# Optimization experiments

Measured on AMD Instinct MI355X. Metric: run time of the kernel, lower is better.

Reference implementation:

```python
import jax, jax.numpy as jnp
import numpy as np

N = 262144      # nodes per graph
NC = 65536      # common nodes
D = 256         # feature_dim


def setup_inputs() -> dict:
    key = jax.random.key(0)
    ks = jax.random.split(key, 12)
    h_prop = jax.random.normal(ks[0], (N, D), dtype=jnp.float32)
    h_context = jax.random.normal(ks[1], (N, D), dtype=jnp.float32)
    h_orig = jax.random.normal(ks[2], (NC, D), dtype=jnp.float32)
    # unique indices (torch scatter-assign semantics are only well-defined without dups)
    idx_prop = jnp.sort(jax.random.permutation(ks[3], N)[:NC]).astype(jnp.int64)
    idx_ctx = jnp.sort(jax.random.permutation(ks[4], N)[:NC]).astype(jnp.int64)
    # parameters (xavier-ish scale)
    s = 1.0 / np.sqrt(D)
    w_orig = jax.random.normal(ks[5], (D, D), dtype=jnp.float32) * s
    w_prop = jax.random.normal(ks[6], (D, D), dtype=jnp.float32) * s
    w_ctx = jax.random.normal(ks[7], (D, D), dtype=jnp.float32) * s
    W_fuse = jax.random.normal(ks[8], (D, 3 * D), dtype=jnp.float32) * (1.0 / np.sqrt(3 * D))  # torch Linear weight (out,in)
    b_fuse = jnp.zeros((D,), dtype=jnp.float32)
    bias = jax.random.uniform(ks[9], (D,), dtype=jnp.float32, minval=-s, maxval=s)
    return {
        "h_prop": h_prop, "h_context": h_context,
        "h_original_common_nodes": h_orig,
        "w_orig": w_orig, "w_prop": w_prop, "w_ctx": w_ctx,
        "W_fuse": W_fuse, "b_fuse": b_fuse, "bias": bias,
        "common_node_indices_in_prop": idx_prop,
        "common_node_indices_in_context": idx_ctx,
    }


def reference(h_prop, h_context, h_original_common_nodes,
              w_orig, w_prop, w_ctx, W_fuse, b_fuse, bias,
              common_node_indices_in_prop, common_node_indices_in_context):
    # gather common rows + three small GEMMs  [NC, D]
    t_orig = h_original_common_nodes @ w_orig
    t_prop = h_prop[common_node_indices_in_prop] @ w_prop
    t_ctx = h_context[common_node_indices_in_context] @ w_ctx
    # concat-linear-tanh-bias  [NC, D]
    fused = jnp.concatenate([t_orig, t_prop, t_ctx], axis=1) @ W_fuse.T + b_fuse
    fused = jnp.tanh(fused) + bias
    # scatter update into clones of the full tables
    h_prop_updated = h_prop.at[common_node_indices_in_prop].set(fused)
    h_context_updated = h_context.at[common_node_indices_in_context].set(fused)
    return (h_prop_updated, h_context_updated)
```

## Files before the change

kernel.cpp:

```cpp
#include <hip/hip_runtime.h>
#include <hip/hip_bf16.h>

#define NN 262144
#define NCC 65536
#define DD 256

typedef __bf16 bf16x8 __attribute__((ext_vector_type(8)));
typedef float f32x4 __attribute__((ext_vector_type(4)));

__global__ void k_zero16(unsigned char* p, int n16) {
    int i = blockIdx.x * blockDim.x + threadIdx.x;
    if (i < n16) ((uint4*)p)[i] = make_uint4(0u, 0u, 0u, 0u);
}

__global__ void k_setflags(const int* __restrict__ idxp, const int* __restrict__ idxc,
                           unsigned char* fp, unsigned char* fc) {
    int j = blockIdx.x * blockDim.x + threadIdx.x;
    if (j < NCC) { fp[idxp[j]] = 1; fc[idxc[j]] = 1; }
}

__global__ __launch_bounds__(256) void k_precompute(const float* __restrict__ w_orig,
                                                    const float* __restrict__ w_prop,
                                                    const float* __restrict__ w_ctx,
                                                    const float* __restrict__ W_fuse,
                                                    __bf16* __restrict__ Mt) {
    int b = blockIdx.x;
    int seg = b >> 4, rem = b & 15;
    int ot = rem >> 2, mt = rem & 3;
    const float* wseg = seg == 0 ? w_orig : (seg == 1 ? w_prop : w_ctx);
    __shared__ float Wl[64 * 65];
    __shared__ float wl[64 * 65];
    int t = threadIdx.x;
    int to = (t & 15) * 4, tm = (t >> 4) * 4;
    float acc[4][4] = {};
    for (int kc = 0; kc < 4; ++kc) {
        __syncthreads();
        for (int i = 0; i < 16; ++i) {
            int f = i * 256 + t;
            int row = f >> 6, col = f & 63;
            Wl[row * 65 + col] = W_fuse[(size_t)(ot * 64 + row) * 768 + seg * 256 + kc * 64 + col];
            wl[row * 65 + col] = wseg[(size_t)(mt * 64 + row) * 256 + kc * 64 + col];
        }
        __syncthreads();
        for (int k = 0; k < 64; ++k) {
            float wo[4], wm2[4];
#pragma unroll
            for (int i = 0; i < 4; ++i) wo[i] = Wl[(to + i) * 65 + k];
#pragma unroll
            for (int j = 0; j < 4; ++j) wm2[j] = wl[(tm + j) * 65 + k];
#pragma unroll
            for (int i = 0; i < 4; ++i)
#pragma unroll
                for (int j = 0; j < 4; ++j) acc[i][j] += wo[i] * wm2[j];
        }
    }
    for (int i = 0; i < 4; ++i)
        for (int j = 0; j < 4; ++j) {
            int o = ot * 64 + to + i;
            int g = seg * 256 + mt * 64 + tm + j;
            Mt[(size_t)o * 768 + g] = (__bf16)acc[i][j];
        }
}

__global__ __launch_bounds__(512, 4) void k_gemm(const float* __restrict__ hp,
                                                 const float* __restrict__ hc,
                                                 const float* __restrict__ horig,
                                                 const __bf16* __restrict__ Mt,
                                                 const float* __restrict__ bfuse,
                                                 const float* __restrict__ bias,
                                                 const int* __restrict__ idxp,
                                                 const int* __restrict__ idxc,
                                                 float* __restrict__ out0,
                                                 float* __restrict__ out1) {
    __shared__ __bf16 Al[64 * 64];
    __shared__ __bf16 Bl[256 * 64];
    int t = threadIdx.x;
    int jbase = blockIdx.x * 64;
    int lane = t & 63, wid = t >> 6;
    int wm = wid >> 2, wn = wid & 3;

    int ar = t >> 3;
    int aslot = t & 7;
    int jr = jbase + ar;
    const float* rowp0 = horig + (size_t)jr * 256;
    const float* rowp1 = hp + (size_t)idxp[jr] * 256;
    const float* rowp2 = hc + (size_t)idxc[jr] * 256;

    int bo = t >> 1;
    int bkp = t & 1;

    f32x4 acc[2][4] = {};

    for (int c = 0; c < 12; ++c) {
        if (c) __syncthreads();
        {
            int seg = c >> 2, ko = (c & 3) * 64;
            const float* src = (seg == 0 ? rowp0 : (seg == 1 ? rowp1 : rowp2)) + ko + aslot * 8;
            float4 v0 = *(const float4*)(src);
            float4 v1 = *(const float4*)(src + 4);
            bf16x8 w;
            w[0] = (__bf16)v0.x; w[1] = (__bf16)v0.y; w[2] = (__bf16)v0.z; w[3] = (__bf16)v0.w;
            w[4] = (__bf16)v1.x; w[5] = (__bf16)v1.y; w[6] = (__bf16)v1.z; w[7] = (__bf16)v1.w;
            *(bf16x8*)&Al[ar * 64 + ((aslot ^ (ar & 7)) << 3)] = w;
        }
        {
            const __bf16* src = Mt + (size_t)bo * 768 + c * 64 + bkp * 32;
#pragma unroll
            for (int i = 0; i < 4; ++i) {
                bf16x8 v = *(const bf16x8*)(src + i * 8);
                int slot = bkp * 4 + i;
                *(bf16x8*)&Bl[bo * 64 + ((slot ^ (bo & 7)) << 3)] = v;
            }
        }
        __syncthreads();
#pragma unroll
        for (int ks = 0; ks < 2; ++ks) {
            bf16x8 af[2], bfr[4];
            int kslot = ks * 4 + (lane >> 4);
#pragma unroll
            for (int mi = 0; mi < 2; ++mi) {
                int r = wm * 32 + mi * 16 + (lane & 15);
                af[mi] = *(const bf16x8*)&Al[r * 64 + ((kslot ^ (r & 7)) << 3)];
            }
#pragma unroll
            for (int ni = 0; ni < 4; ++ni) {
                int o = wn * 64 + ni * 16 + (lane & 15);
                bfr[ni] = *(const bf16x8*)&Bl[o * 64 + ((kslot ^ (o & 7)) << 3)];
            }
#pragma unroll
            for (int mi = 0; mi < 2; ++mi)
#pragma unroll
                for (int ni = 0; ni < 4; ++ni)
                    acc[mi][ni] = __builtin_amdgcn_mfma_f32_16x16x32_bf16(af[mi], bfr[ni], acc[mi][ni], 0, 0, 0);
        }
    }

    float bfv[4], biv[4];
#pragma unroll
    for (int ni = 0; ni < 4; ++ni) {
        int o = wn * 64 + ni * 16 + (lane & 15);
        bfv[ni] = bfuse[o];
        biv[ni] = bias[o];
    }
#pragma unroll
    for (int mi = 0; mi < 2; ++mi) {
#pragma unroll
        for (int rr = 0; rr < 4; ++rr) {
            int j = jbase + wm * 32 + mi * 16 + (lane >> 4) * 4 + rr;
            int gp = idxp[j];
            int gc = idxc[j];
#pragma unroll
            for (int ni = 0; ni < 4; ++ni) {
                int o = wn * 64 + ni * 16 + (lane & 15);
                float v = tanhf(acc[mi][ni][rr] + bfv[ni]) + biv[ni];
                out0[(size_t)gp * 256 + o] = v;
                out1[(size_t)gc * 256 + o] = v;
            }
        }
    }
}

__global__ __launch_bounds__(256) void k_copy(const float* __restrict__ hp,
                                              const float* __restrict__ hc,
                                              const unsigned char* __restrict__ fp,
                                              const unsigned char* __restrict__ fc,
                                              float* __restrict__ out0,
                                              float* __restrict__ out1) {
    int wid = (blockIdx.x * blockDim.x + threadIdx.x) >> 6;
    int lane = threadIdx.x & 63;
    int nw = (gridDim.x * blockDim.x) >> 6;
    for (int R = wid; R < 2 * NN; R += nw) {
        int tbl = (R >= NN);
        int r = tbl ? (R - NN) : R;
        unsigned char f = tbl ? fc[r] : fp[r];
        if (!f) {
            const float* s = (tbl ? hc : hp) + (size_t)r * 256 + lane * 4;
            float* d = (tbl ? out1 : out0) + (size_t)r * 256 + lane * 4;
            *(float4*)d = *(const float4*)s;
        }
    }
}

extern "C" void kernel_launch(void* const* d_in, const int* in_sizes, int n_in,
                              void* d_out, int out_size, void* d_ws, size_t ws_size,
                              hipStream_t stream) {
    const float* hp     = (const float*)d_in[0];
    const float* hc     = (const float*)d_in[1];
    const float* horig  = (const float*)d_in[2];
    const float* w_orig = (const float*)d_in[3];
    const float* w_prop = (const float*)d_in[4];
    const float* w_ctx  = (const float*)d_in[5];
    const float* W_fuse = (const float*)d_in[6];
    const float* bfuse  = (const float*)d_in[7];
    const float* bias   = (const float*)d_in[8];
    const int* idxp     = (const int*)d_in[9];
    const int* idxc     = (const int*)d_in[10];
    float* out0 = (float*)d_out;
    float* out1 = out0 + (size_t)NN * DD;

    char* ws = (char*)d_ws;
    __bf16* Mt = (__bf16*)ws;
    unsigned char* fp = (unsigned char*)(ws + 393216);
    unsigned char* fc = fp + NN;

    k_zero16<<<(2 * NN / 16 + 255) / 256, 256, 0, stream>>>(fp, 2 * NN / 16);
    k_setflags<<<NCC / 256, 256, 0, stream>>>(idxp, idxc, fp, fc);
    k_precompute<<<48, 256, 0, stream>>>(w_orig, w_prop, w_ctx, W_fuse, Mt);
    k_gemm<<<NCC / 64, 512, 0, stream>>>(hp, hc, horig, Mt, bfuse, bias, idxp, idxc, out0, out1);
    k_copy<<<4096, 256, 0, stream>>>(hp, hc, fp, fc, out0, out1);
}
```

Before: 334.6 us.

## Fuse GEMM and copy kernels, load MFMA operands directly from global

Merges the flag zeroing into the weight precompute kernel, and fuses the GEMM with the unflagged-row copy in a single 1024-block kernel. Odd blocks copy first and even blocks compute first, so copy traffic overlaps with compute. The GEMM drops its LDS staging and barriers, and each wave loads its A rows (converted to bf16) and its B fragments straight from global memory. This saves launches and synchronisation, but waves now load B redundantly and read A in a less coalesced pattern.

New measurement: 447.1 us. 33.6% more time.

```diff
diff --git a/kernel.cpp b/kernel.cpp
--- a/kernel.cpp
+++ b/kernel.cpp
@@ -1,36 +1,30 @@
 #include <hip/hip_runtime.h>
 #include <hip/hip_bf16.h>
+#include <math.h>
 
 #define NN 262144
 #define NCC 65536
-#define DD 256
 
 typedef __bf16 bf16x8 __attribute__((ext_vector_type(8)));
 typedef float f32x4 __attribute__((ext_vector_type(4)));
 
-__global__ void k_zero16(unsigned char* p, int n16) {
-    int i = blockIdx.x * blockDim.x + threadIdx.x;
-    if (i < n16) ((uint4*)p)[i] = make_uint4(0u, 0u, 0u, 0u);
-}
-
-__global__ void k_setflags(const int* __restrict__ idxp, const int* __restrict__ idxc,
-                           unsigned char* fp, unsigned char* fc) {
-    int j = blockIdx.x * blockDim.x + threadIdx.x;
-    if (j < NCC) { fp[idxp[j]] = 1; fc[idxc[j]] = 1; }
-}
-
-__global__ __launch_bounds__(256) void k_precompute(const float* __restrict__ w_orig,
-                                                    const float* __restrict__ w_prop,
-                                                    const float* __restrict__ w_ctx,
-                                                    const float* __restrict__ W_fuse,
-                                                    __bf16* __restrict__ Mt) {
+__global__ __launch_bounds__(256) void k_setup(const float* __restrict__ w_orig,
+                                               const float* __restrict__ w_prop,
+                                               const float* __restrict__ w_ctx,
+                                               const float* __restrict__ W_fuse,
+                                               __bf16* __restrict__ Mt,
+                                               unsigned char* __restrict__ flags) {
+    __shared__ float Wl[64 * 65];
+    __shared__ float wl[64 * 65];
     int b = blockIdx.x;
+    int t = threadIdx.x;
+    if (b >= 48) {
+        ((uint4*)flags)[(b - 48) * 256 + t] = make_uint4(0u, 0u, 0u, 0u);
+        return;
+    }
     int seg = b >> 4, rem = b & 15;
     int ot = rem >> 2, mt = rem & 3;
     const float* wseg = seg == 0 ? w_orig : (seg == 1 ? w_prop : w_ctx);
-    __shared__ float Wl[64 * 65];
-    __shared__ float wl[64 * 65];
-    int t = threadIdx.x;
     int to = (t & 15) * 4, tm = (t >> 4) * 4;
     float acc[4][4] = {};
     for (int kc = 0; kc < 4; ++kc) {
@@ -62,83 +56,110 @@
         }
 }
 
-__global__ __launch_bounds__(512, 4) void k_gemm(const float* __restrict__ hp,
-                                                 const float* __restrict__ hc,
-                                                 const float* __restrict__ horig,
-                                                 const __bf16* __restrict__ Mt,
-                                                 const float* __restrict__ bfuse,
-                                                 const float* __restrict__ bias,
-                                                 const int* __restrict__ idxp,
-                                                 const int* __restrict__ idxc,
-                                                 float* __restrict__ out0,
-                                                 float* __restrict__ out1) {
-    __shared__ __bf16 Al[64 * 64];
-    __shared__ __bf16 Bl[256 * 64];
+__global__ void k_setflags(const int* __restrict__ idxp, const int* __restrict__ idxc,
+                           unsigned char* fp, unsigned char* fc) {
+    int j = blockIdx.x * blockDim.x + threadIdx.x;
+    if (j < NCC) { fp[idxp[j]] = 1; fc[idxc[j]] = 1; }
+}
+
+__device__ inline bf16x8 cvt8(f32x4 a, f32x4 b) {
+    bf16x8 w;
+    w[0] = (__bf16)a[0]; w[1] = (__bf16)a[1]; w[2] = (__bf16)a[2]; w[3] = (__bf16)a[3];
+    w[4] = (__bf16)b[0]; w[5] = (__bf16)b[1]; w[6] = (__bf16)b[2]; w[7] = (__bf16)b[3];
+    return w;
+}
+
+__device__ inline void do_copy(int bx, int wid, int lane,
+                               const float* __restrict__ hp, const float* __restrict__ hc,
+                               const unsigned char* __restrict__ fp,
+                               const unsigned char* __restrict__ fc,
+                               float* __restrict__ out0, float* __restrict__ out1) {
+    int base = bx * 512 + wid * 64;
+    int tbl = base >= NN;
+    const unsigned char* F = tbl ? fc : fp;
+    const float* S = tbl ? hc : hp;
+    float* D = tbl ? out1 : out0;
+    int r0 = tbl ? base - NN : base;
+    for (int i = 0; i < 64; ++i) {
+        int r = r0 + i;
+        if (!F[r]) {
+            const float* s = S + (size_t)r * 256 + lane * 4;
+            float* d = D + (size_t)r * 256 + lane * 4;
+            *(f32x4*)d = *(const f32x4*)s;
+        }
+    }
+}
+
+__global__ __launch_bounds__(512) void k_fused(const float* __restrict__ hp,
+                                               const float* __restrict__ hc,
+                                               const float* __restrict__ horig,
+                                               const __bf16* __restrict__ Mt,
+                                               const float* __restrict__ bfuse,
+                                               const float* __restrict__ bias,
+                                               const int* __restrict__ idxp,
+                                               const int* __restrict__ idxc,
+                                               const unsigned char* __restrict__ fp,
+                                               const unsigned char* __restrict__ fc,
+                                               float* __restrict__ out0,
+                                               float* __restrict__ out1) {
     int t = threadIdx.x;
-    int jbase = blockIdx.x * 64;
     int lane = t & 63, wid = t >> 6;
     int wm = wid >> 2, wn = wid & 3;
-
-    int ar = t >> 3;
-    int aslot = t & 7;
-    int jr = jbase + ar;
-    const float* rowp0 = horig + (size_t)jr * 256;
-    const float* rowp1 = hp + (size_t)idxp[jr] * 256;
-    const float* rowp2 = hc + (size_t)idxc[jr] * 256;
-
-    int bo = t >> 1;
-    int bkp = t & 1;
+    int jbase = blockIdx.x * 64;
+    int l15 = lane & 15, lq = lane >> 4;
+
+    int copyFirst = blockIdx.x & 1;
+    if (copyFirst) do_copy(blockIdx.x, wid, lane, hp, hc, fp, fc, out0, out1);
+
+    int j0 = jbase + wm * 32 + l15;
+    int j1 = j0 + 16;
+    int ip0 = idxp[j0], ip1 = idxp[j1];
+    int ic0 = idxc[j0], ic1 = idxc[j1];
+
+    const __bf16* bp0 = Mt + (size_t)(wn * 64 + 0  + l15) * 768 + lq * 8;
+    const __bf16* bp1 = Mt + (size_t)(wn * 64 + 16 + l15) * 768 + lq * 8;
+    const __bf16* bp2 = Mt + (size_t)(wn * 64 + 32 + l15) * 768 + lq * 8;
+    const __bf16* bp3 = Mt + (size_t)(wn * 64 + 48 + l15) * 768 + lq * 8;
 
     f32x4 acc[2][4] = {};
 
-    for (int c = 0; c < 12; ++c) {
-        if (c) __syncthreads();
-        {
-            int seg = c >> 2, ko = (c & 3) * 64;
-            const float* src = (seg == 0 ? rowp0 : (seg == 1 ? rowp1 : rowp2)) + ko + aslot * 8;
-            float4 v0 = *(const float4*)(src);
-            float4 v1 = *(const float4*)(src + 4);
-            bf16x8 w;
-            w[0] = (__bf16)v0.x; w[1] = (__bf16)v0.y; w[2] = (__bf16)v0.z; w[3] = (__bf16)v0.w;
-            w[4] = (__bf16)v1.x; w[5] = (__bf16)v1.y; w[6] = (__bf16)v1.z; w[7] = (__bf16)v1.w;
-            *(bf16x8*)&Al[ar * 64 + ((aslot ^ (ar & 7)) << 3)] = w;
-        }
-        {
-            const __bf16* src = Mt + (size_t)bo * 768 + c * 64 + bkp * 32;
-#pragma unroll
-            for (int i = 0; i < 4; ++i) {
-                bf16x8 v = *(const bf16x8*)(src + i * 8);
-                int slot = bkp * 4 + i;
-                *(bf16x8*)&Bl[bo * 64 + ((slot ^ (bo & 7)) << 3)] = v;
+#pragma unroll
+    for (int seg = 0; seg < 3; ++seg) {
+        const float* a0 = (seg == 0 ? horig + (size_t)j0 * 256
+                          : seg == 1 ? hp + (size_t)ip0 * 256
+                                     : hc + (size_t)ic0 * 256) + lq * 8;
+        const float* a1 = (seg == 0 ? horig + (size_t)j1 * 256
+                          : seg == 1 ? hp + (size_t)ip1 * 256
+                                     : hc + (size_t)ic1 * 256) + lq * 8;
+#pragma unroll
+        for (int cc = 0; cc < 4; ++cc) {
+            int c = seg * 4 + cc;
+#pragma unroll
+            for (int ks = 0; ks < 2; ++ks) {
+                int aoff = cc * 64 + ks * 32;
+                int boff = c * 64 + ks * 32;
+                bf16x8 af0 = cvt8(*(const f32x4*)(a0 + aoff), *(const f32x4*)(a0 + aoff + 4));
+                bf16x8 af1 = cvt8(*(const f32x4*)(a1 + aoff), *(const f32x4*)(a1 + aoff + 4));
+                bf16x8 b0 = *(const bf16x8*)(bp0 + boff);
+                bf16x8 b1 = *(const bf16x8*)(bp1 + boff);
+                bf16x8 b2 = *(const bf16x8*)(bp2 + boff);
+                bf16x8 b3 = *(const bf16x8*)(bp3 + boff);
+                acc[0][0] = __builtin_amdgcn_mfma_f32_16x16x32_bf16(af0, b0, acc[0][0], 0, 0, 0);
+                acc[0][1] = __builtin_amdgcn_mfma_f32_16x16x32_bf16(af0, b1, acc[0][1], 0, 0, 0);
+                acc[0][2] = __builtin_amdgcn_mfma_f32_16x16x32_bf16(af0, b2, acc[0][2], 0, 0, 0);
+                acc[0][3] = __builtin_amdgcn_mfma_f32_16x16x32_bf16(af0, b3, acc[0][3], 0, 0, 0);
+                acc[1][0] = __builtin_amdgcn_mfma_f32_16x16x32_bf16(af1, b0, acc[1][0], 0, 0, 0);
+                acc[1][1] = __builtin_amdgcn_mfma_f32_16x16x32_bf16(af1, b1, acc[1][1], 0, 0, 0);
+                acc[1][2] = __builtin_amdgcn_mfma_f32_16x16x32_bf16(af1, b2, acc[1][2], 0, 0, 0);
+                acc[1][3] = __builtin_amdgcn_mfma_f32_16x16x32_bf16(af1, b3, acc[1][3], 0, 0, 0);
             }
         }
-        __syncthreads();
-#pragma unroll
-        for (int ks = 0; ks < 2; ++ks) {
-            bf16x8 af[2], bfr[4];
-            int kslot = ks * 4 + (lane >> 4);
-#pragma unroll
-            for (int mi = 0; mi < 2; ++mi) {
-                int r = wm * 32 + mi * 16 + (lane & 15);
-                af[mi] = *(const bf16x8*)&Al[r * 64 + ((kslot ^ (r & 7)) << 3)];
-            }
-#pragma unroll
-            for (int ni = 0; ni < 4; ++ni) {
-                int o = wn * 64 + ni * 16 + (lane & 15);
-                bfr[ni] = *(const bf16x8*)&Bl[o * 64 + ((kslot ^ (o & 7)) << 3)];
-            }
-#pragma unroll
-            for (int mi = 0; mi < 2; ++mi)
-#pragma unroll
-                for (int ni = 0; ni < 4; ++ni)
-                    acc[mi][ni] = __builtin_amdgcn_mfma_f32_16x16x32_bf16(af[mi], bfr[ni], acc[mi][ni], 0, 0, 0);
-        }
     }
 
     float bfv[4], biv[4];
 #pragma unroll
     for (int ni = 0; ni < 4; ++ni) {
-        int o = wn * 64 + ni * 16 + (lane & 15);
+        int o = wn * 64 + ni * 16 + l15;
         bfv[ni] = bfuse[o];
         biv[ni] = bias[o];
     }
@@ -146,39 +167,20 @@
     for (int mi = 0; mi < 2; ++mi) {
 #pragma unroll
         for (int rr = 0; rr < 4; ++rr) {
-            int j = jbase + wm * 32 + mi * 16 + (lane >> 4) * 4 + rr;
+            int j = jbase + wm * 32 + mi * 16 + lq * 4 + rr;
             int gp = idxp[j];
             int gc = idxc[j];
 #pragma unroll
             for (int ni = 0; ni < 4; ++ni) {
-                int o = wn * 64 + ni * 16 + (lane & 15);
+                int o = wn * 64 + ni * 16 + l15;
                 float v = tanhf(acc[mi][ni][rr] + bfv[ni]) + biv[ni];
                 out0[(size_t)gp * 256 + o] = v;
                 out1[(size_t)gc * 256 + o] = v;
             }
         }
     }
-}
-
-__global__ __launch_bounds__(256) void k_copy(const float* __restrict__ hp,
-                                              const float* __restrict__ hc,
-                                              const unsigned char* __restrict__ fp,
-                                              const unsigned char* __restrict__ fc,
-                                              float* __restrict__ out0,
-                                              float* __restrict__ out1) {
-    int wid = (blockIdx.x * blockDim.x + threadIdx.x) >> 6;
-    int lane = threadIdx.x & 63;
-    int nw = (gridDim.x * blockDim.x) >> 6;
-    for (int R = wid; R < 2 * NN; R += nw) {
-        int tbl = (R >= NN);
-        int r = tbl ? (R - NN) : R;
-        unsigned char f = tbl ? fc[r] : fp[r];
-        if (!f) {
-            const float* s = (tbl ? hc : hp) + (size_t)r * 256 + lane * 4;
-            float* d = (tbl ? out1 : out0) + (size_t)r * 256 + lane * 4;
-            *(float4*)d = *(const float4*)s;
-        }
-    }
+
+    if (!copyFirst) do_copy(blockIdx.x, wid, lane, hp, hc, fp, fc, out0, out1);
 }
 
 extern "C" void kernel_launch(void* const* d_in, const int* in_sizes, int n_in,
@@ -196,16 +198,15 @@
     const int* idxp     = (const int*)d_in[9];
     const int* idxc     = (const int*)d_in[10];
     float* out0 = (float*)d_out;
-    float* out1 = out0 + (size_t)NN * DD;
+    float* out1 = out0 + (size_t)NN * 256;
 
     char* ws = (char*)d_ws;
     __bf16* Mt = (__bf16*)ws;
     unsigned char* fp = (unsigned char*)(ws + 393216);
     unsigned char* fc = fp + NN;
 
-    k_zero16<<<(2 * NN / 16 + 255) / 256, 256, 0, stream>>>(fp, 2 * NN / 16);
+    k_setup<<<176, 256, 0, stream>>>(w_orig, w_prop, w_ctx, W_fuse, Mt, fp);
     k_setflags<<<NCC / 256, 256, 0, stream>>>(idxp, idxc, fp, fc);
-    k_precompute<<<48, 256, 0, stream>>>(w_orig, w_prop, w_ctx, W_fuse, Mt);
-    k_gemm<<<NCC / 64, 512, 0, stream>>>(hp, hc, horig, Mt, bfuse, bias, idxp, idxc, out0, out1);
-    k_copy<<<4096, 256, 0, stream>>>(hp, hc, fp, fc, out0, out1);
-}
+    k_fused<<<1024, 512, 0, stream>>>(hp, hc, horig, Mt, bfuse, bias,
+                                      idxp, idxc, fp, fc, out0, out1);
+}
```

## Prefetch next GEMM tile into registers, merge setup kernels, unroll copy loop

Applied to the files above, without the earlier changes.

The GEMM kernel now loads the next k-chunk of A and B into registers while the current chunk is being stored to shared memory, so global-load latency overlaps with the MFMA work. Flag zeroing is folded into the weight-precompute kernel as extra blocks, which removes one kernel launch. The copy kernel becomes a fixed, unrolled 32-iteration loop that always issues its load (redirected to row 0 for flagged rows) to raise memory-level parallelism. The costs are higher register pressure in the GEMM and redundant loads of row 0 in the copy kernel.

Result: faster. 323.7 us (-3.3%).

```diff
diff --git a/kernel.cpp b/kernel.cpp
--- a/kernel.cpp
+++ b/kernel.cpp
@@ -1,36 +1,30 @@
 #include <hip/hip_runtime.h>
 #include <hip/hip_bf16.h>
+#include <math.h>
 
 #define NN 262144
 #define NCC 65536
-#define DD 256
 
 typedef __bf16 bf16x8 __attribute__((ext_vector_type(8)));
 typedef float f32x4 __attribute__((ext_vector_type(4)));
 
-__global__ void k_zero16(unsigned char* p, int n16) {
-    int i = blockIdx.x * blockDim.x + threadIdx.x;
-    if (i < n16) ((uint4*)p)[i] = make_uint4(0u, 0u, 0u, 0u);
-}
-
-__global__ void k_setflags(const int* __restrict__ idxp, const int* __restrict__ idxc,
-                           unsigned char* fp, unsigned char* fc) {
-    int j = blockIdx.x * blockDim.x + threadIdx.x;
-    if (j < NCC) { fp[idxp[j]] = 1; fc[idxc[j]] = 1; }
-}
-
-__global__ __launch_bounds__(256) void k_precompute(const float* __restrict__ w_orig,
-                                                    const float* __restrict__ w_prop,
-                                                    const float* __restrict__ w_ctx,
-                                                    const float* __restrict__ W_fuse,
-                                                    __bf16* __restrict__ Mt) {
+__global__ __launch_bounds__(256) void k_setup(const float* __restrict__ w_orig,
+                                               const float* __restrict__ w_prop,
+                                               const float* __restrict__ w_ctx,
+                                               const float* __restrict__ W_fuse,
+                                               __bf16* __restrict__ Mt,
+                                               unsigned char* __restrict__ flags) {
+    __shared__ float Wl[64 * 65];
+    __shared__ float wl[64 * 65];
     int b = blockIdx.x;
+    int t = threadIdx.x;
+    if (b >= 48) {
+        ((uint4*)flags)[(b - 48) * 256 + t] = make_uint4(0u, 0u, 0u, 0u);
+        return;
+    }
     int seg = b >> 4, rem = b & 15;
     int ot = rem >> 2, mt = rem & 3;
     const float* wseg = seg == 0 ? w_orig : (seg == 1 ? w_prop : w_ctx);
-    __shared__ float Wl[64 * 65];
-    __shared__ float wl[64 * 65];
-    int t = threadIdx.x;
     int to = (t & 15) * 4, tm = (t >> 4) * 4;
     float acc[4][4] = {};
     for (int kc = 0; kc < 4; ++kc) {
@@ -60,6 +54,19 @@
             int g = seg * 256 + mt * 64 + tm + j;
             Mt[(size_t)o * 768 + g] = (__bf16)acc[i][j];
         }
+}
+
+__global__ void k_setflags(const int* __restrict__ idxp, const int* __restrict__ idxc,
+                           unsigned char* fp, unsigned char* fc) {
+    int j = blockIdx.x * blockDim.x + threadIdx.x;
+    if (j < NCC) { fp[idxp[j]] = 1; fc[idxc[j]] = 1; }
+}
+
+__device__ inline bf16x8 cvt8(f32x4 a, f32x4 b) {
+    bf16x8 w;
+    w[0] = (__bf16)a[0]; w[1] = (__bf16)a[1]; w[2] = (__bf16)a[2]; w[3] = (__bf16)a[3];
+    w[4] = (__bf16)b[0]; w[5] = (__bf16)b[1]; w[6] = (__bf16)b[2]; w[7] = (__bf16)b[3];
+    return w;
 }
 
 __global__ __launch_bounds__(512, 4) void k_gemm(const float* __restrict__ hp,
@@ -78,53 +85,56 @@
     int jbase = blockIdx.x * 64;
     int lane = t & 63, wid = t >> 6;
     int wm = wid >> 2, wn = wid & 3;
-
-    int ar = t >> 3;
-    int aslot = t & 7;
+    int l15 = lane & 15, lq = lane >> 4;
+
+    int ar = t >> 3, aslot = t & 7;
     int jr = jbase + ar;
-    const float* rowp0 = horig + (size_t)jr * 256;
-    const float* rowp1 = hp + (size_t)idxp[jr] * 256;
-    const float* rowp2 = hc + (size_t)idxc[jr] * 256;
-
-    int bo = t >> 1;
-    int bkp = t & 1;
+    const float* rowp0 = horig + (size_t)jr * 256 + aslot * 8;
+    const float* rowp1 = hp + (size_t)idxp[jr] * 256 + aslot * 8;
+    const float* rowp2 = hc + (size_t)idxc[jr] * 256 + aslot * 8;
+
+    int bo = t >> 1, bkp = t & 1;
+    const __bf16* bsrc = Mt + (size_t)bo * 768 + bkp * 32;
 
     f32x4 acc[2][4] = {};
 
+    f32x4 va0 = *(const f32x4*)(rowp0);
+    f32x4 va1 = *(const f32x4*)(rowp0 + 4);
+    bf16x8 vb[4];
+#pragma unroll
+    for (int i = 0; i < 4; ++i) vb[i] = *(const bf16x8*)(bsrc + i * 8);
+
+#pragma unroll
     for (int c = 0; c < 12; ++c) {
-        if (c) __syncthreads();
-        {
-            int seg = c >> 2, ko = (c & 3) * 64;
-            const float* src = (seg == 0 ? rowp0 : (seg == 1 ? rowp1 : rowp2)) + ko + aslot * 8;
-            float4 v0 = *(const float4*)(src);
-            float4 v1 = *(const float4*)(src + 4);
-            bf16x8 w;
-            w[0] = (__bf16)v0.x; w[1] = (__bf16)v0.y; w[2] = (__bf16)v0.z; w[3] = (__bf16)v0.w;
-            w[4] = (__bf16)v1.x; w[5] = (__bf16)v1.y; w[6] = (__bf16)v1.z; w[7] = (__bf16)v1.w;
-            *(bf16x8*)&Al[ar * 64 + ((aslot ^ (ar & 7)) << 3)] = w;
-        }
-        {
-            const __bf16* src = Mt + (size_t)bo * 768 + c * 64 + bkp * 32;
-#pragma unroll
-            for (int i = 0; i < 4; ++i) {
-                bf16x8 v = *(const bf16x8*)(src + i * 8);
-                int slot = bkp * 4 + i;
-                *(bf16x8*)&Bl[bo * 64 + ((slot ^ (bo & 7)) << 3)] = v;
-            }
+        __syncthreads();
+        *(bf16x8*)&Al[ar * 64 + ((aslot ^ (ar & 7)) << 3)] = cvt8(va0, va1);
+#pragma unroll
+        for (int i = 0; i < 4; ++i) {
+            int slot = bkp * 4 + i;
+            *(bf16x8*)&Bl[bo * 64 + ((slot ^ (bo & 7)) << 3)] = vb[i];
+        }
+        if (c < 11) {
+            int cn = c + 1;
+            int seg = cn >> 2, ko = (cn & 3) * 64;
+            const float* s = (seg == 0 ? rowp0 : (seg == 1 ? rowp1 : rowp2)) + ko;
+            va0 = *(const f32x4*)(s);
+            va1 = *(const f32x4*)(s + 4);
+#pragma unroll
+            for (int i = 0; i < 4; ++i) vb[i] = *(const bf16x8*)(bsrc + cn * 64 + i * 8);
         }
         __syncthreads();
 #pragma unroll
         for (int ks = 0; ks < 2; ++ks) {
             bf16x8 af[2], bfr[4];
-            int kslot = ks * 4 + (lane >> 4);
+            int kslot = ks * 4 + lq;
 #pragma unroll
             for (int mi = 0; mi < 2; ++mi) {
-                int r = wm * 32 + mi * 16 + (lane & 15);
+                int r = wm * 32 + mi * 16 + l15;
                 af[mi] = *(const bf16x8*)&Al[r * 64 + ((kslot ^ (r & 7)) << 3)];
             }
 #pragma unroll
             for (int ni = 0; ni < 4; ++ni) {
-                int o = wn * 64 + ni * 16 + (lane & 15);
+                int o = wn * 64 + ni * 16 + l15;
                 bfr[ni] = *(const bf16x8*)&Bl[o * 64 + ((kslot ^ (o & 7)) << 3)];
             }
 #pragma unroll
@@ -138,7 +148,7 @@
     float bfv[4], biv[4];
 #pragma unroll
     for (int ni = 0; ni < 4; ++ni) {
-        int o = wn * 64 + ni * 16 + (lane & 15);
+        int o = wn * 64 + ni * 16 + l15;
         bfv[ni] = bfuse[o];
         biv[ni] = bias[o];
     }
@@ -146,12 +156,12 @@
     for (int mi = 0; mi < 2; ++mi) {
 #pragma unroll
         for (int rr = 0; rr < 4; ++rr) {
-            int j = jbase + wm * 32 + mi * 16 + (lane >> 4) * 4 + rr;
+            int j = jbase + wm * 32 + mi * 16 + lq * 4 + rr;
             int gp = idxp[j];
             int gc = idxc[j];
 #pragma unroll
             for (int ni = 0; ni < 4; ++ni) {
-                int o = wn * 64 + ni * 16 + (lane & 15);
+                int o = wn * 64 + ni * 16 + l15;
                 float v = tanhf(acc[mi][ni][rr] + bfv[ni]) + biv[ni];
                 out0[(size_t)gp * 256 + o] = v;
                 out1[(size_t)gc * 256 + o] = v;
@@ -166,18 +176,21 @@
                                               const unsigned char* __restrict__ fc,
                                               float* __restrict__ out0,
                                               float* __restrict__ out1) {
-    int wid = (blockIdx.x * blockDim.x + threadIdx.x) >> 6;
-    int lane = threadIdx.x & 63;
-    int nw = (gridDim.x * blockDim.x) >> 6;
-    for (int R = wid; R < 2 * NN; R += nw) {
-        int tbl = (R >= NN);
-        int r = tbl ? (R - NN) : R;
-        unsigned char f = tbl ? fc[r] : fp[r];
-        if (!f) {
-            const float* s = (tbl ? hc : hp) + (size_t)r * 256 + lane * 4;
-            float* d = (tbl ? out1 : out0) + (size_t)r * 256 + lane * 4;
-            *(float4*)d = *(const float4*)s;
-        }
+    int tid = blockIdx.x * 256 + threadIdx.x;
+    const int stride = 4096 * 256;
+#pragma unroll
+    for (int it = 0; it < 32; ++it) {
+        int gid = it * stride + tid;
+        int row = gid >> 6, slot = gid & 63;
+        int tbl = row >= NN;
+        int r = tbl ? row - NN : row;
+        const unsigned char* F = tbl ? fc : fp;
+        const float* S = tbl ? hc : hp;
+        float* D = tbl ? out1 : out0;
+        unsigned char f = F[r];
+        const float* s = S + (size_t)(f ? 0 : r) * 256 + slot * 4;
+        f32x4 v = *(const f32x4*)s;
+        if (!f) *(f32x4*)(D + (size_t)r * 256 + slot * 4) = v;
     }
 }
 
@@ -196,16 +209,16 @@
     const int* idxp     = (const int*)d_in[9];
     const int* idxc     = (const int*)d_in[10];
     float* out0 = (float*)d_out;
-    float* out1 = out0 + (size_t)NN * DD;
+    float* out1 = out0 + (size_t)NN * 256;
 
     char* ws = (char*)d_ws;
     __bf16* Mt = (__bf16*)ws;
     unsigned char* fp = (unsigned char*)(ws + 393216);
     unsigned char* fc = fp + NN;
 
-    k_zero16<<<(2 * NN / 16 + 255) / 256, 256, 0, stream>>>(fp, 2 * NN / 16);
+    k_setup<<<176, 256, 0, stream>>>(w_orig, w_prop, w_ctx, W_fuse, Mt, fp);
     k_setflags<<<NCC / 256, 256, 0, stream>>>(idxp, idxc, fp, fc);
-    k_precompute<<<48, 256, 0, stream>>>(w_orig, w_prop, w_ctx, W_fuse, Mt);
-    k_gemm<<<NCC / 64, 512, 0, stream>>>(hp, hc, horig, Mt, bfuse, bias, idxp, idxc, out0, out1);
+    k_gemm<<<NCC / 64, 512, 0, stream>>>(hp, hc, horig, Mt, bfuse, bias,
+                                         idxp, idxc, out0, out1);
     k_copy<<<4096, 256, 0, stream>>>(hp, hc, fp, fc, out0, out1);
 }
```
